# Performance work log

Hardware: AMD Instinct MI355X
Metric: run time of the kernel (lower is better)

The kernel has to match this reference:

```python
import jax, jax.numpy as jnp
import numpy as np

# Module config (matches init_kwargs)
DIM = 256
NUM_HEADS = 8
AREA = 4
B, C, H, W = 8, DIM, 64, 64
HEAD_DIM = DIM // NUM_HEADS

# Each Conv in the source is Conv2d(bias=False) + BatchNorm2d + Identity (activation=False).
# In eval mode BN is a per-channel affine, so we represent each Conv as (weight, scale, bias).

def setup_inputs() -> dict:
    key = jax.random.key(0)
    ks = jax.random.split(key, 13)
    def w(k, shape, s=0.05):
        return jax.random.normal(k, shape, jnp.float32) * s
    def bn_scale(k, n):
        return 1.0 + 0.02 * jax.random.normal(k, (n,), jnp.float32)
    x = jax.random.normal(ks[0], (B, C, H, W), jnp.float32)
    return {
        "x": x,
        "w_qk": w(ks[1], (2 * C, C)),        # 1x1 conv: [out,in]
        "s_qk": bn_scale(ks[2], 2 * C),
        "b_qk": w(ks[3], (2 * C,), 0.01),
        "w_v": w(ks[4], (C, C)),
        "s_v": bn_scale(ks[5], C),
        "b_v": w(ks[6], (C,), 0.01),
        "w_pe": w(ks[7], (C, 1, 5, 5)),       # depthwise 5x5, groups=C
        "s_pe": bn_scale(ks[8], C),
        "b_pe": w(ks[9], (C,), 0.01),
        "w_proj": w(ks[10], (C, C)),
        "s_proj": bn_scale(ks[11], C),
        "b_proj": w(ks[12], (C,), 0.01),
    }


def _affine(y, s, b):
    # per-channel BN-eval affine on NCHW
    return y * s[None, :, None, None] + b[None, :, None, None]


def _conv1x1(x, w, s, b):
    return _affine(jnp.einsum('bchw,oc->bohw', x, w), s, b)


def reference(x, w_qk, s_qk, b_qk, w_v, s_v, b_v, w_pe, s_pe, b_pe, w_proj, s_proj, b_proj):
    N = H * W
    Na = N // AREA
    Ba = B * AREA

    qk = _conv1x1(x, w_qk, s_qk, b_qk)                    # [B, 2C, H, W]
    v4 = _conv1x1(x, w_v, s_v, b_v)                       # [B, C, H, W]
    pp = _affine(
        jax.lax.conv_general_dilated(
            v4, w_pe, (1, 1), 'SAME', feature_group_count=C,
            dimension_numbers=('NCHW', 'OIHW', 'NCHW')),
        s_pe, b_pe)                                        # [B, C, H, W]

    # flatten(2).transpose(1,2) then area split along N
    qk = qk.reshape(B, 2 * C, N).transpose(0, 2, 1).reshape(Ba, Na, 2 * C)
    v = v4.reshape(B, C, N).transpose(0, 2, 1).reshape(Ba, Na, C)

    q = qk[..., :C].reshape(Ba, Na, NUM_HEADS, HEAD_DIM)
    k = qk[..., C:].reshape(Ba, Na, NUM_HEADS, HEAD_DIM)
    vh = v.reshape(Ba, Na, NUM_HEADS, HEAD_DIM)

    scale = jnp.asarray(HEAD_DIM, jnp.float32) ** -0.5
    attn = jnp.einsum('bqhd,bkhd->bhqk', q, k) * scale     # [Ba, h, Na, Na]
    attn = jax.nn.softmax(attn, axis=-1)                   # max-stable softmax over keys
    o = jnp.einsum('bhqk,bkhd->bqhd', attn, vh)            # [Ba, Na, h, d]
    o = o.reshape(Ba, Na, C).reshape(B, N, C)
    o = o.reshape(B, H, W, C).transpose(0, 3, 1, 2)        # [B, C, H, W]

    return _conv1x1(o + pp, w_proj, s_proj, b_proj)
```

## Files before the change

kernel.cpp:

```cpp
#include <hip/hip_runtime.h>
#include <math.h>


#define NN 4096
#define NA 1024

typedef unsigned short us;
typedef __attribute__((ext_vector_type(4))) unsigned short us4;
typedef __attribute__((ext_vector_type(8))) unsigned short us8;
typedef __attribute__((ext_vector_type(8))) short bf16x8;
typedef __attribute__((ext_vector_type(4))) float f32x4;

#define QS (0.17677669529663687f * 1.4426950408889634f)

__device__ __forceinline__ us f2b(float f) {
    unsigned u = __builtin_bit_cast(unsigned, f);
    u += 0x7fffu + ((u >> 16) & 1u);
    return (us)(u >> 16);
}
__device__ __forceinline__ float b2f(us h) {
    unsigned u = ((unsigned)h) << 16;
    return __builtin_bit_cast(float, u);
}
__device__ __forceinline__ unsigned pack2(float lo, float hi) {
    return (unsigned)f2b(lo) | ((unsigned)f2b(hi) << 16);
}
__device__ __forceinline__ unsigned cvtpk_bf16(float lo, float hi) {
    unsigned r;
    asm("v_cvt_pk_bf16_f32 %0, %1, %2" : "=v"(r) : "v"(lo), "v"(hi));
    return r;
}
__device__ __forceinline__ float fexp2(float x) {
    float r;
    asm("v_exp_f32 %0, %1" : "=v"(r) : "v"(x));
    return r;
}

__device__ __forceinline__ size_t wswz(int ch, int k) {
    return ((size_t)((ch >> 4) * 8 + (k >> 5))) * 512 + ((((k >> 3) & 3) * 16 + (ch & 15))) * 8 + (k & 7);
}

__global__ __launch_bounds__(256) void prep_kernel(
    const float* __restrict__ w_qk, const float* __restrict__ s_qk, const float* __restrict__ b_qk,
    const float* __restrict__ w_v,  const float* __restrict__ s_v,
    const float* __restrict__ w_proj, const float* __restrict__ s_proj,
    us* __restrict__ wqkh, us* __restrict__ wvh, us* __restrict__ wprojh,
    float* __restrict__ bqkp)
{
    int idx = blockIdx.x * 256 + threadIdx.x;
    if (idx < 131072) {
        int o = idx >> 8, k = idx & 255;
        float sc = s_qk[o] * (o < 256 ? QS : 1.0f);
        wqkh[wswz(o, k)] = f2b(w_qk[idx] * sc);
    } else if (idx < 196608) {
        int j = idx - 131072; int o = j >> 8, k = j & 255;
        wvh[wswz(o, k)] = f2b(w_v[j] * s_v[o]);
    } else {
        int j = idx - 196608; int o = j >> 8, k = j & 255;
        wprojh[wswz(o, k)] = f2b(w_proj[j] * s_proj[o]);
    }
    if (idx < 512) bqkp[idx] = b_qk[idx] * (idx < 256 ? QS : 1.0f);
}

__global__ __launch_bounds__(256) void qkv_kernel(
    const float* __restrict__ x,
    const us* __restrict__ wqkh, const float* __restrict__ bqkp,
    const us* __restrict__ wvh,  const float* __restrict__ b_v,
    us* __restrict__ qt, us* __restrict__ vbuf)
{
    const int n0 = blockIdx.x * 64;
    const int b  = blockIdx.y;
    const int tid = threadIdx.x;
    const int w = tid >> 6, lane = tid & 63, c = lane & 15, g = lane >> 4;

    __shared__ __align__(16) us Xs[64][264];

    const float* Xb = x + (size_t)b * 256 * NN;
    #pragma unroll
    for (int i = 0; i < 16; i++) {
        int t = tid + i * 256;
        int cp = t >> 5, pp = t & 31;
        const float* r0 = Xb + (size_t)(2 * cp) * NN + n0 + 2 * pp;
        float2 a0 = *(const float2*)r0;
        float2 a1 = *(const float2*)(r0 + NN);
        *(unsigned*)&Xs[2 * pp][2 * cp]     = pack2(a0.x, a1.x);
        *(unsigned*)&Xs[2 * pp + 1][2 * cp] = pack2(a0.y, a1.y);
    }
    __syncthreads();

    for (int grp = 0; grp < 3; grp++) {
        f32x4 acc[4][4] = {};
        for (int kc = 0; kc < 256; kc += 32) {
            bf16x8 Xf[4];
            #pragma unroll
            for (int j = 0; j < 4; j++)
                Xf[j] = *(const bf16x8*)&Xs[j * 16 + c][kc + g * 8];
            #pragma unroll
            for (int cgi = 0; cgi < 4; cgi++) {
                int chbase = (grp < 2 ? (grp * 4 + cgi) * 64 : cgi * 64);
                const us* Wp = (grp < 2 ? wqkh : wvh) +
                    ((size_t)(((chbase >> 4) + w) * 8 + (kc >> 5))) * 512 + lane * 8;
                bf16x8 Wf = *(const bf16x8*)Wp;
                if (grp < 2) {
                    #pragma unroll
                    for (int j = 0; j < 4; j++)
                        acc[cgi][j] = __builtin_amdgcn_mfma_f32_16x16x32_bf16(Xf[j], Wf, acc[cgi][j], 0, 0, 0);
                } else {
                    #pragma unroll
                    for (int j = 0; j < 4; j++)
                        acc[cgi][j] = __builtin_amdgcn_mfma_f32_16x16x32_bf16(Wf, Xf[j], acc[cgi][j], 0, 0, 0);
                }
            }
        }
        if (grp < 2) {
            #pragma unroll
            for (int cgi = 0; cgi < 4; cgi++) {
                int ch = (grp * 4 + cgi) * 64 + w * 16 + c;
                float bb = bqkp[ch];
                #pragma unroll
                for (int j = 0; j < 4; j++)
                    #pragma unroll
                    for (int r = 0; r < 4; r++)
                        qt[((size_t)b * 4096 + n0 + j * 16 + g * 4 + r) * 512 + ch] =
                            f2b(acc[cgi][j][r] + bb);
            }
        } else {
            #pragma unroll
            for (int cgi = 0; cgi < 4; cgi++)
                #pragma unroll
                for (int r = 0; r < 4; r++) {
                    int ch = cgi * 64 + w * 16 + g * 4 + r;
                    float bb = b_v[ch];
                    #pragma unroll
                    for (int j = 0; j < 4; j++)
                        vbuf[((size_t)b * 256 + ch) * NN + n0 + j * 16 + c] =
                            f2b(acc[cgi][j][r] + bb);
                }
        }
    }
}

__global__ __launch_bounds__(256) void pe_conv_kernel(
    const us* __restrict__ vbuf,
    const float* __restrict__ w_pe, const float* __restrict__ s_pe, const float* __restrict__ b_pe,
    float* __restrict__ opp)
{
    const int c = blockIdx.x, b = blockIdx.y;
    const int tid = threadIdx.x;
    const us* vp = vbuf + ((size_t)b * 256 + c) * NN;
    __shared__ float plane[4096];
    __shared__ float wloc[25];
    #pragma unroll
    for (int i = 0; i < 4; i++) {
        int idx = tid + i * 256;
        us4 v = *(const us4*)&vp[idx * 4];
        float4 f;
        f.x = b2f(v[0]); f.y = b2f(v[1]); f.z = b2f(v[2]); f.w = b2f(v[3]);
        *(float4*)&plane[idx * 4] = f;
    }
    if (tid < 25) wloc[tid] = w_pe[c * 25 + tid];
    __syncthreads();

    const float s = s_pe[c], bb = b_pe[c];
    float* op = opp + ((size_t)b * 256 + c) * NN;
    for (int i = 0; i < 16; i++) {
        int pix = tid + i * 256;
        int ph = pix >> 6, pw = pix & 63;
        float acc = 0.f;
        #pragma unroll
        for (int dy = -2; dy <= 2; dy++) {
            int hy = ph + dy;
            if (hy < 0 || hy > 63) continue;
            #pragma unroll
            for (int dx = -2; dx <= 2; dx++) {
                int wx = pw + dx;
                if (wx < 0 || wx > 63) continue;
                acc += plane[hy * 64 + wx] * wloc[(dy + 2) * 5 + (dx + 2)];
            }
        }
        op[pix] = acc * s + bb;
    }
}

__global__ __launch_bounds__(256) void attn_kernel(
    const us* __restrict__ qt, const us* __restrict__ vbuf, float* __restrict__ opp)
{
    const int h   = blockIdx.x;
    const int qtb = blockIdx.y;
    const int ba  = blockIdx.z;
    const int b = ba >> 2, a = ba & 3;
    const int tid = threadIdx.x;
    const int w = tid >> 6, lane = tid & 63, c = lane & 15, g = lane >> 4;
    const int q0 = qtb * 128;

    __shared__ __align__(16) us Kt[2][64][40];
    __shared__ __align__(16) us Vs[2][2048];
    __shared__ __align__(16) us Ps[128][72];

    const int krow = tid >> 2, kseg = tid & 3;
    const int vrow = tid >> 3, vseg = tid & 7;
    const int vbyte = vrow * 128 + ((vseg ^ (vrow & 7)) << 4);

    const us* Kg = qt + ((size_t)b * 4096 + a * NA) * 512 + 256 + h * 32;
    const us* Vg = vbuf + ((size_t)b * 256 + h * 32) * NN + a * NA;

    const us* Qp = qt + ((size_t)b * 4096 + a * NA + q0 + w * 16 + c) * 512 + h * 32 + g * 8;
    const bf16x8 Qf0 = *(const bf16x8*)Qp;
    const bf16x8 Qf1 = *(const bf16x8*)(Qp + (size_t)64 * 512);

    {
        us8 kreg = *(const us8*)(Kg + (size_t)krow * 512 + kseg * 8);
        us8 vreg = *(const us8*)(Vg + (size_t)vrow * NN + vseg * 8);
        *(us8*)&Kt[0][krow][kseg * 8] = kreg;
        *(us8*)((char*)Vs[0] + vbyte) = vreg;
    }
    __syncthreads();

    const bf16x8 ones = {0x3F80, 0x3F80, 0x3F80, 0x3F80, 0x3F80, 0x3F80, 0x3F80, 0x3F80};
    const f32x4 z = {0.f, 0.f, 0.f, 0.f};
    const int qr0 = w * 16 + c, qr1 = 64 + w * 16 + c;

    f32x4 O0a = z, O1a = z, Osa = z;
    f32x4 O0b = z, O1b = z, Osb = z;
    int cur = 0;

    for (int kt = 0; kt < 16; kt++) {
        us8 kreg, vreg;
        if (kt < 15) {
            const int kv1 = (kt + 1) * 64;
            kreg = *(const us8*)(Kg + ((size_t)(kv1 + krow)) * 512 + kseg * 8);
            vreg = *(const us8*)(Vg + (size_t)vrow * NN + kv1 + vseg * 8);
        }

        f32x4 sA[4], sB[4];
        #pragma unroll
        for (int j = 0; j < 4; j++) {
            bf16x8 Kf = *(const bf16x8*)&Kt[cur][j * 16 + c][g * 8];
            sA[j] = __builtin_amdgcn_mfma_f32_16x16x32_bf16(Kf, Qf0, z, 0, 0, 0);
            sB[j] = __builtin_amdgcn_mfma_f32_16x16x32_bf16(Kf, Qf1, z, 0, 0, 0);
        }

        #pragma unroll
        for (int j = 0; j < 4; j++) {
            uint2 pr;
            pr.x = cvtpk_bf16(fexp2(sA[j][0]), fexp2(sA[j][1]));
            pr.y = cvtpk_bf16(fexp2(sA[j][2]), fexp2(sA[j][3]));
            *(uint2*)&Ps[qr0][j * 16 + g * 4] = pr;
        }
        asm volatile("s_waitcnt lgkmcnt(0)" ::: "memory");
        __builtin_amdgcn_sched_barrier(0);

        uint2 prb[4];
        #pragma unroll
        for (int j = 0; j < 4; j++) {
            prb[j].x = cvtpk_bf16(fexp2(sB[j][0]), fexp2(sB[j][1]));
            prb[j].y = cvtpk_bf16(fexp2(sB[j][2]), fexp2(sB[j][3]));
        }

        #pragma unroll
        for (int ks = 0; ks < 2; ks++) {
            int so = (((ks * 4 + g) ^ (c & 7)) << 4);
            bf16x8 Bv0 = *(const bf16x8*)((char*)Vs[cur] + c * 128 + so);
            bf16x8 Bv1 = *(const bf16x8*)((char*)Vs[cur] + (16 + c) * 128 + so);
            bf16x8 Ap0 = *(const bf16x8*)&Ps[qr0][ks * 32 + g * 8];
            O0a = __builtin_amdgcn_mfma_f32_16x16x32_bf16(Ap0, Bv0, O0a, 0, 0, 0);
            O1a = __builtin_amdgcn_mfma_f32_16x16x32_bf16(Ap0, Bv1, O1a, 0, 0, 0);
            Osa = __builtin_amdgcn_mfma_f32_16x16x32_bf16(Ap0, ones, Osa, 0, 0, 0);
        }

        #pragma unroll
        for (int j = 0; j < 4; j++)
            *(uint2*)&Ps[qr1][j * 16 + g * 4] = prb[j];
        asm volatile("s_waitcnt lgkmcnt(0)" ::: "memory");
        __builtin_amdgcn_sched_barrier(0);

        #pragma unroll
        for (int ks = 0; ks < 2; ks++) {
            int so = (((ks * 4 + g) ^ (c & 7)) << 4);
            bf16x8 Bv0 = *(const bf16x8*)((char*)Vs[cur] + c * 128 + so);
            bf16x8 Bv1 = *(const bf16x8*)((char*)Vs[cur] + (16 + c) * 128 + so);
            bf16x8 Ap1 = *(const bf16x8*)&Ps[qr1][ks * 32 + g * 8];
            O0b = __builtin_amdgcn_mfma_f32_16x16x32_bf16(Ap1, Bv0, O0b, 0, 0, 0);
            O1b = __builtin_amdgcn_mfma_f32_16x16x32_bf16(Ap1, Bv1, O1b, 0, 0, 0);
            Osb = __builtin_amdgcn_mfma_f32_16x16x32_bf16(Ap1, ones, Osb, 0, 0, 0);
        }

        if (kt < 15) {
            *(us8*)&Kt[cur ^ 1][krow][kseg * 8] = kreg;
            *(us8*)((char*)Vs[cur ^ 1] + vbyte) = vreg;
        }
        __syncthreads();
        cur ^= 1;
    }

    float linva[4], linvb[4];
    #pragma unroll
    for (int r = 0; r < 4; r++) { linva[r] = 1.0f / Osa[r]; linvb[r] = 1.0f / Osb[r]; }

    float* Ob = opp + ((size_t)(b * 256 + h * 32)) * NN + a * NA + q0 + w * 16 + g * 4;
    {
        float4 o = *(float4*)(Ob + (size_t)c * NN);
        o.x += O0a[0] * linva[0]; o.y += O0a[1] * linva[1];
        o.z += O0a[2] * linva[2]; o.w += O0a[3] * linva[3];
        *(float4*)(Ob + (size_t)c * NN) = o;
        float4 o2 = *(float4*)(Ob + (size_t)(16 + c) * NN);
        o2.x += O1a[0] * linva[0]; o2.y += O1a[1] * linva[1];
        o2.z += O1a[2] * linva[2]; o2.w += O1a[3] * linva[3];
        *(float4*)(Ob + (size_t)(16 + c) * NN) = o2;

        float* Ob2 = Ob + 64;
        float4 o3 = *(float4*)(Ob2 + (size_t)c * NN);
        o3.x += O0b[0] * linvb[0]; o3.y += O0b[1] * linvb[1];
        o3.z += O0b[2] * linvb[2]; o3.w += O0b[3] * linvb[3];
        *(float4*)(Ob2 + (size_t)c * NN) = o3;
        float4 o4 = *(float4*)(Ob2 + (size_t)(16 + c) * NN);
        o4.x += O1b[0] * linvb[0]; o4.y += O1b[1] * linvb[1];
        o4.z += O1b[2] * linvb[2]; o4.w += O1b[3] * linvb[3];
        *(float4*)(Ob2 + (size_t)(16 + c) * NN) = o4;
    }
}

__global__ __launch_bounds__(256) void proj_kernel(
    const float* __restrict__ opp,
    const us* __restrict__ wprojh, const float* __restrict__ b_proj,
    float* __restrict__ out)
{
    const int n0 = blockIdx.x * 64;
    const int b  = blockIdx.y;
    const int tid = threadIdx.x;
    const int w = tid >> 6, lane = tid & 63, c = lane & 15, g = lane >> 4;

    __shared__ __align__(16) us Xs[64][264];

    const float* Xb = opp + (size_t)b * 256 * NN;
    #pragma unroll
    for (int i = 0; i < 16; i++) {
        int t = tid + i * 256;
        int cp = t >> 5, pp = t & 31;
        const float* r0 = Xb + (size_t)(2 * cp) * NN + n0 + 2 * pp;
        float2 a0 = *(const float2*)r0;
        float2 a1 = *(const float2*)(r0 + NN);
        *(unsigned*)&Xs[2 * pp][2 * cp]     = pack2(a0.x, a1.x);
        *(unsigned*)&Xs[2 * pp + 1][2 * cp] = pack2(a0.y, a1.y);
    }
    __syncthreads();

    f32x4 acc[4][4] = {};
    for (int kc = 0; kc < 256; kc += 32) {
        bf16x8 Xf[4];
        #pragma unroll
        for (int j = 0; j < 4; j++)
            Xf[j] = *(const bf16x8*)&Xs[j * 16 + c][kc + g * 8];
        #pragma unroll
        for (int cgi = 0; cgi < 4; cgi++) {
            const us* Wp = wprojh +
                ((size_t)((cgi * 4 + w) * 8 + (kc >> 5))) * 512 + lane * 8;
            bf16x8 Wf = *(const bf16x8*)Wp;
            #pragma unroll
            for (int j = 0; j < 4; j++)
                acc[cgi][j] = __builtin_amdgcn_mfma_f32_16x16x32_bf16(Wf, Xf[j], acc[cgi][j], 0, 0, 0);
        }
    }

    #pragma unroll
    for (int cgi = 0; cgi < 4; cgi++)
        #pragma unroll
        for (int r = 0; r < 4; r++) {
            int ch = cgi * 64 + w * 16 + g * 4 + r;
            float bb = b_proj[ch];
            #pragma unroll
            for (int j = 0; j < 4; j++)
                out[((size_t)b * 256 + ch) * NN + n0 + j * 16 + c] = acc[cgi][j][r] + bb;
        }
}

extern "C" void kernel_launch(void* const* d_in, const int* in_sizes, int n_in,
                              void* d_out, int out_size, void* d_ws, size_t ws_size,
                              hipStream_t stream) {
    const float* x      = (const float*)d_in[0];
    const float* w_qk   = (const float*)d_in[1];
    const float* s_qk   = (const float*)d_in[2];
    const float* b_qk   = (const float*)d_in[3];
    const float* w_v    = (const float*)d_in[4];
    const float* s_v    = (const float*)d_in[5];
    const float* b_v    = (const float*)d_in[6];
    const float* w_pe   = (const float*)d_in[7];
    const float* s_pe   = (const float*)d_in[8];
    const float* b_pe   = (const float*)d_in[9];
    const float* w_proj = (const float*)d_in[10];
    const float* s_proj = (const float*)d_in[11];
    const float* b_proj = (const float*)d_in[12];
    float* out = (float*)d_out;

    char* p = (char*)d_ws;
    us* qtb     = (us*)p;                  p += (size_t)8 * 4096 * 512 * 2;
    us* vbuf    = (us*)p;                  p += (size_t)8 * 256 * 4096 * 2;
    float* opp  = (float*)p;               p += (size_t)8 * 256 * 4096 * 4;
    us* wqkh    = (us*)p;                  p += (size_t)512 * 256 * 2;
    us* wvh     = (us*)p;                  p += (size_t)256 * 256 * 2;
    us* wprojh  = (us*)p;                  p += (size_t)256 * 256 * 2;
    float* bqkp = (float*)p;

    prep_kernel<<<1024, 256, 0, stream>>>(w_qk, s_qk, b_qk, w_v, s_v,
                                          w_proj, s_proj, wqkh, wvh, wprojh, bqkp);
    qkv_kernel<<<dim3(64, 8), 256, 0, stream>>>(x, wqkh, bqkp, wvh, b_v, qtb, vbuf);
    pe_conv_kernel<<<dim3(256, 8), 256, 0, stream>>>(vbuf, w_pe, s_pe, b_pe, opp);
    attn_kernel<<<dim3(8, 8, 32), 256, 0, stream>>>(qtb, vbuf, opp);
    proj_kernel<<<dim3(64, 8), 256, 0, stream>>>(opp, wprojh, b_proj, out);
}
```

Measured before the change: 155.8 us.

## Store pe/attention intermediate in bf16 and halve qkv tile width

The pe-conv output buffer that attention accumulates into and proj reads is changed from fp32 to bf16, halving its traffic across three kernels. The proj loader now packs bf16 pairs directly instead of converting floats. Separately, the qkv kernel uses 32-pixel tiles instead of 64, doubling the grid for more parallelism at the cost of more weight reloads. Storing the intermediate in bf16 adds rounding, since the attention output is added to an already-rounded value and rounded again.

```diff
diff --git a/kernel.cpp b/kernel.cpp
--- a/kernel.cpp
+++ b/kernel.cpp
@@ -68,18 +68,18 @@
     const us* __restrict__ wvh,  const float* __restrict__ b_v,
     us* __restrict__ qt, us* __restrict__ vbuf)
 {
-    const int n0 = blockIdx.x * 64;
+    const int n0 = blockIdx.x * 32;
     const int b  = blockIdx.y;
     const int tid = threadIdx.x;
     const int w = tid >> 6, lane = tid & 63, c = lane & 15, g = lane >> 4;
 
-    __shared__ __align__(16) us Xs[64][264];
+    __shared__ __align__(16) us Xs[32][264];
 
     const float* Xb = x + (size_t)b * 256 * NN;
     #pragma unroll
-    for (int i = 0; i < 16; i++) {
+    for (int i = 0; i < 8; i++) {
         int t = tid + i * 256;
-        int cp = t >> 5, pp = t & 31;
+        int cp = t >> 4, pp = t & 15;
         const float* r0 = Xb + (size_t)(2 * cp) * NN + n0 + 2 * pp;
         float2 a0 = *(const float2*)r0;
         float2 a1 = *(const float2*)(r0 + NN);
@@ -89,11 +89,11 @@
     __syncthreads();
 
     for (int grp = 0; grp < 3; grp++) {
-        f32x4 acc[4][4] = {};
+        f32x4 acc[4][2] = {};
         for (int kc = 0; kc < 256; kc += 32) {
-            bf16x8 Xf[4];
-            #pragma unroll
-            for (int j = 0; j < 4; j++)
+            bf16x8 Xf[2];
+            #pragma unroll
+            for (int j = 0; j < 2; j++)
                 Xf[j] = *(const bf16x8*)&Xs[j * 16 + c][kc + g * 8];
             #pragma unroll
             for (int cgi = 0; cgi < 4; cgi++) {
@@ -103,11 +103,11 @@
                 bf16x8 Wf = *(const bf16x8*)Wp;
                 if (grp < 2) {
                     #pragma unroll
-                    for (int j = 0; j < 4; j++)
+                    for (int j = 0; j < 2; j++)
                         acc[cgi][j] = __builtin_amdgcn_mfma_f32_16x16x32_bf16(Xf[j], Wf, acc[cgi][j], 0, 0, 0);
                 } else {
                     #pragma unroll
-                    for (int j = 0; j < 4; j++)
+                    for (int j = 0; j < 2; j++)
                         acc[cgi][j] = __builtin_amdgcn_mfma_f32_16x16x32_bf16(Wf, Xf[j], acc[cgi][j], 0, 0, 0);
                 }
             }
@@ -118,7 +118,7 @@
                 int ch = (grp * 4 + cgi) * 64 + w * 16 + c;
                 float bb = bqkp[ch];
                 #pragma unroll
-                for (int j = 0; j < 4; j++)
+                for (int j = 0; j < 2; j++)
                     #pragma unroll
                     for (int r = 0; r < 4; r++)
                         qt[((size_t)b * 4096 + n0 + j * 16 + g * 4 + r) * 512 + ch] =
@@ -132,7 +132,7 @@
                     int ch = cgi * 64 + w * 16 + g * 4 + r;
                     float bb = b_v[ch];
                     #pragma unroll
-                    for (int j = 0; j < 4; j++)
+                    for (int j = 0; j < 2; j++)
                         vbuf[((size_t)b * 256 + ch) * NN + n0 + j * 16 + c] =
                             f2b(acc[cgi][j][r] + bb);
                 }
@@ -143,7 +143,7 @@
 __global__ __launch_bounds__(256) void pe_conv_kernel(
     const us* __restrict__ vbuf,
     const float* __restrict__ w_pe, const float* __restrict__ s_pe, const float* __restrict__ b_pe,
-    float* __restrict__ opp)
+    us* __restrict__ opp)
 {
     const int c = blockIdx.x, b = blockIdx.y;
     const int tid = threadIdx.x;
@@ -162,7 +162,7 @@
     __syncthreads();
 
     const float s = s_pe[c], bb = b_pe[c];
-    float* op = opp + ((size_t)b * 256 + c) * NN;
+    us* op = opp + ((size_t)b * 256 + c) * NN;
     for (int i = 0; i < 16; i++) {
         int pix = tid + i * 256;
         int ph = pix >> 6, pw = pix & 63;
@@ -178,12 +178,12 @@
                 acc += plane[hy * 64 + wx] * wloc[(dy + 2) * 5 + (dx + 2)];
             }
         }
-        op[pix] = acc * s + bb;
+        op[pix] = f2b(acc * s + bb);
     }
 }
 
 __global__ __launch_bounds__(256) void attn_kernel(
-    const us* __restrict__ qt, const us* __restrict__ vbuf, float* __restrict__ opp)
+    const us* __restrict__ qt, const us* __restrict__ vbuf, us* __restrict__ opp)
 {
     const int h   = blockIdx.x;
     const int qtb = blockIdx.y;
@@ -297,31 +297,31 @@
     #pragma unroll
     for (int r = 0; r < 4; r++) { linva[r] = 1.0f / Osa[r]; linvb[r] = 1.0f / Osb[r]; }
 
-    float* Ob = opp + ((size_t)(b * 256 + h * 32)) * NN + a * NA + q0 + w * 16 + g * 4;
+    us* Ob = opp + ((size_t)(b * 256 + h * 32)) * NN + a * NA + q0 + w * 16 + g * 4;
     {
-        float4 o = *(float4*)(Ob + (size_t)c * NN);
-        o.x += O0a[0] * linva[0]; o.y += O0a[1] * linva[1];
-        o.z += O0a[2] * linva[2]; o.w += O0a[3] * linva[3];
-        *(float4*)(Ob + (size_t)c * NN) = o;
-        float4 o2 = *(float4*)(Ob + (size_t)(16 + c) * NN);
-        o2.x += O1a[0] * linva[0]; o2.y += O1a[1] * linva[1];
-        o2.z += O1a[2] * linva[2]; o2.w += O1a[3] * linva[3];
-        *(float4*)(Ob + (size_t)(16 + c) * NN) = o2;
-
-        float* Ob2 = Ob + 64;
-        float4 o3 = *(float4*)(Ob2 + (size_t)c * NN);
-        o3.x += O0b[0] * linvb[0]; o3.y += O0b[1] * linvb[1];
-        o3.z += O0b[2] * linvb[2]; o3.w += O0b[3] * linvb[3];
-        *(float4*)(Ob2 + (size_t)c * NN) = o3;
-        float4 o4 = *(float4*)(Ob2 + (size_t)(16 + c) * NN);
-        o4.x += O1b[0] * linvb[0]; o4.y += O1b[1] * linvb[1];
-        o4.z += O1b[2] * linvb[2]; o4.w += O1b[3] * linvb[3];
-        *(float4*)(Ob2 + (size_t)(16 + c) * NN) = o4;
+        us4 o = *(us4*)(Ob + (size_t)c * NN);
+        #pragma unroll
+        for (int r = 0; r < 4; r++) o[r] = f2b(b2f(o[r]) + O0a[r] * linva[r]);
+        *(us4*)(Ob + (size_t)c * NN) = o;
+        us4 o2 = *(us4*)(Ob + (size_t)(16 + c) * NN);
+        #pragma unroll
+        for (int r = 0; r < 4; r++) o2[r] = f2b(b2f(o2[r]) + O1a[r] * linva[r]);
+        *(us4*)(Ob + (size_t)(16 + c) * NN) = o2;
+
+        us* Ob2 = Ob + 64;
+        us4 o3 = *(us4*)(Ob2 + (size_t)c * NN);
+        #pragma unroll
+        for (int r = 0; r < 4; r++) o3[r] = f2b(b2f(o3[r]) + O0b[r] * linvb[r]);
+        *(us4*)(Ob2 + (size_t)c * NN) = o3;
+        us4 o4 = *(us4*)(Ob2 + (size_t)(16 + c) * NN);
+        #pragma unroll
+        for (int r = 0; r < 4; r++) o4[r] = f2b(b2f(o4[r]) + O1b[r] * linvb[r]);
+        *(us4*)(Ob2 + (size_t)(16 + c) * NN) = o4;
     }
 }
 
 __global__ __launch_bounds__(256) void proj_kernel(
-    const float* __restrict__ opp,
+    const us* __restrict__ opp,
     const us* __restrict__ wprojh, const float* __restrict__ b_proj,
     float* __restrict__ out)
 {
@@ -332,16 +332,15 @@
 
     __shared__ __align__(16) us Xs[64][264];
 
-    const float* Xb = opp + (size_t)b * 256 * NN;
+    const us* Xb = opp + (size_t)b * 256 * NN;
     #pragma unroll
     for (int i = 0; i < 16; i++) {
         int t = tid + i * 256;
         int cp = t >> 5, pp = t & 31;
-        const float* r0 = Xb + (size_t)(2 * cp) * NN + n0 + 2 * pp;
-        float2 a0 = *(const float2*)r0;
-        float2 a1 = *(const float2*)(r0 + NN);
-        *(unsigned*)&Xs[2 * pp][2 * cp]     = pack2(a0.x, a1.x);
-        *(unsigned*)&Xs[2 * pp + 1][2 * cp] = pack2(a0.y, a1.y);
+        unsigned a0 = *(const unsigned*)&Xb[(size_t)(2 * cp) * NN + n0 + 2 * pp];
+        unsigned a1 = *(const unsigned*)&Xb[(size_t)(2 * cp + 1) * NN + n0 + 2 * pp];
+        *(unsigned*)&Xs[2 * pp][2 * cp]     = (a0 & 0xFFFFu) | (a1 << 16);
+        *(unsigned*)&Xs[2 * pp + 1][2 * cp] = (a0 >> 16) | (a1 & 0xFFFF0000u);
     }
     __syncthreads();
 
@@ -395,7 +394,7 @@
     char* p = (char*)d_ws;
     us* qtb     = (us*)p;                  p += (size_t)8 * 4096 * 512 * 2;
     us* vbuf    = (us*)p;                  p += (size_t)8 * 256 * 4096 * 2;
-    float* opp  = (float*)p;               p += (size_t)8 * 256 * 4096 * 4;
+    us* opp     = (us*)p;                  p += (size_t)8 * 256 * 4096 * 2;
     us* wqkh    = (us*)p;                  p += (size_t)512 * 256 * 2;
     us* wvh     = (us*)p;                  p += (size_t)256 * 256 * 2;
     us* wprojh  = (us*)p;                  p += (size_t)256 * 256 * 2;
@@ -403,7 +402,7 @@
 
     prep_kernel<<<1024, 256, 0, stream>>>(w_qk, s_qk, b_qk, w_v, s_v,
                                           w_proj, s_proj, wqkh, wvh, wprojh, bqkp);
-    qkv_kernel<<<dim3(64, 8), 256, 0, stream>>>(x, wqkh, bqkp, wvh, b_v, qtb, vbuf);
+    qkv_kernel<<<dim3(128, 8), 256, 0, stream>>>(x, wqkh, bqkp, wvh, b_v, qtb, vbuf);
     pe_conv_kernel<<<dim3(256, 8), 256, 0, stream>>>(vbuf, w_pe, s_pe, b_pe, opp);
     attn_kernel<<<dim3(8, 8, 32), 256, 0, stream>>>(qtb, vbuf, opp);
     proj_kernel<<<dim3(64, 8), 256, 0, stream>>>(opp, wprojh, b_proj, out);
```

New measurement: 177.3 us. 1.14x slower.
